# Optimization experiments

Measured on AMD Instinct MI355X. Metric: run time of the kernel, lower is better.

The kernel has to match this reference:

```python
import jax, jax.numpy as jnp
import numpy as np

TAU = 0.2  # temperature

def setup_inputs() -> dict:
    key = jax.random.key(0)
    k1, k2, k3 = jax.random.split(key, 3)
    query = jax.random.normal(k1, (8192, 128), dtype=jnp.float32)
    pos = jax.random.normal(k2, (8192, 128), dtype=jnp.float32)
    neg = jax.random.normal(k3, (16384, 128), dtype=jnp.float32)
    return {"query": query, "pos": pos, "neg": neg}

def reference(query, pos, neg):
    # scores: [N, M] = query @ neg^T / tau
    scores = jnp.einsum('nd,md->nm', query, neg) / TAU
    # positive logits: [N]
    pos_logit = jnp.sum(query * pos, axis=-1) / TAU
    # loss = mean_n( logsumexp_m(scores) - pos_logit )
    lse = jax.scipy.special.logsumexp(scores, axis=-1)
    return jnp.mean(lse - pos_logit)
```

## Files before the change

### kernel.cpp

```cpp
#include <hip/hip_runtime.h>
#include <cstdint>

#define NQ    8192
#define NNEG  16384
#define DIM   128
#define SPLIT 8
#define CHUNK (NNEG / SPLIT)
#define K_SCALE 7.2134752044448169f
#define LN2     0.69314718055994531f

typedef __attribute__((ext_vector_type(8))) __bf16 bf16x8;
typedef __attribute__((ext_vector_type(4))) float  f32x4;

__device__ inline void async_load16(const void* g, void* l) {
    __builtin_amdgcn_global_load_lds(
        (const __attribute__((address_space(1))) void*)g,
        (__attribute__((address_space(3))) void*)l, 16, 0, 0);
}

__device__ inline unsigned short f2bf(float x) {
    uint32_t u = __float_as_uint(x);
    u += 0x7fffu + ((u >> 16) & 1u);
    return (unsigned short)(u >> 16);
}

__device__ inline float waveReduceSum(float v) {
#pragma unroll
    for (int m = 32; m >= 1; m >>= 1) v += __shfl_xor(v, m, 64);
    return v;
}

__global__ __launch_bounds__(256) void iw_prep(
    const float* __restrict__ q, const float* __restrict__ neg,
    unsigned short* __restrict__ qb, unsigned short* __restrict__ nb,
    float* __restrict__ out)
{
    const int i = blockIdx.x * 256 + threadIdx.x;
    if (i == 0) out[0] = 0.f;
    constexpr int QG = NQ * DIM / 4;
    if (i < QG) {
        float4 v = ((const float4*)q)[i];
        ushort4 o;
        o.x = f2bf(v.x * K_SCALE); o.y = f2bf(v.y * K_SCALE);
        o.z = f2bf(v.z * K_SCALE); o.w = f2bf(v.w * K_SCALE);
        ((ushort4*)qb)[i] = o;
    } else {
        int j = i - QG;
        float4 v = ((const float4*)neg)[j];
        ushort4 o;
        o.x = f2bf(v.x); o.y = f2bf(v.y); o.z = f2bf(v.z); o.w = f2bf(v.w);
        ((ushort4*)nb)[j] = o;
    }
}

__global__ __launch_bounds__(256) void iw_pos(
    const float* __restrict__ q, const float* __restrict__ p,
    float* __restrict__ out)
{
    const int tid = threadIdx.x;
    float acc = 0.f;
    const float4* q4 = (const float4*)q;
    const float4* p4 = (const float4*)p;
    const int n4 = NQ * DIM / 4;
    for (int i = blockIdx.x * 256 + tid; i < n4; i += 128 * 256) {
        float4 a = q4[i], b = p4[i];
        acc = fmaf(a.x, b.x, fmaf(a.y, b.y, fmaf(a.z, b.z, fmaf(a.w, b.w, acc))));
    }
    acc = waveReduceSum(acc);
    __shared__ float red[4];
    if ((tid & 63) == 0) red[tid >> 6] = acc;
    __syncthreads();
    if (tid == 0) {
        float s = red[0] + red[1] + red[2] + red[3];
        atomicAdd(out, s * (-1.0f / (0.2f * (float)NQ)));
    }
}

__global__ __launch_bounds__(256, 2) void iw_main(
    const unsigned short* __restrict__ qb, const unsigned short* __restrict__ nb,
    float2* __restrict__ partial)
{
    constexpr int BM = 128, BN = 64, NIT = CHUNK / BN;
    __shared__ alignas(16) unsigned short q_lds[BM * DIM];
    __shared__ alignas(16) unsigned short n_lds[BN * DIM];

    const int tid  = threadIdx.x;
    const int lane = tid & 63;
    const int w    = tid >> 6;
    const int quad = lane >> 4;
    const int c0   = lane & 15;

    const int row0   = blockIdx.x * BM;
    const int nbase0 = blockIdx.y * CHUNK;

#pragma unroll
    for (int p = 0; p < 8; ++p) {
        int t   = w * 8 + p;
        int idx = t * 64 + lane;
        int r   = idx >> 4;
        int kb  = (idx & 15) ^ (r & 15);
        async_load16(qb + (size_t)(row0 + r) * DIM + kb * 8, q_lds + t * 512);
    }
    int nro[4], ndst[4];
#pragma unroll
    for (int p = 0; p < 4; ++p) {
        int t   = w * 4 + p;
        int idx = t * 64 + lane;
        int r   = idx >> 4;
        int kb  = (idx & 15) ^ (r & 15);
        nro[p]  = r * DIM + kb * 8;
        ndst[p] = t * 512;
        async_load16(nb + (size_t)nbase0 * DIM + nro[p], n_lds + ndst[p]);
    }
    __syncthreads();

    bf16x8 afrag[2][4];
#pragma unroll
    for (int rs = 0; rs < 2; ++rs)
#pragma unroll
        for (int ks = 0; ks < 4; ++ks) {
            int rl  = w * 32 + rs * 16 + c0;
            int blk = rl * 16 + ((ks * 4 + quad) ^ c0);
            afrag[rs][ks] = *reinterpret_cast<const bf16x8*>(q_lds + blk * 8);
        }

    float m_s[2][4], l_s[2][4];
#pragma unroll
    for (int rs = 0; rs < 2; ++rs)
#pragma unroll
        for (int i = 0; i < 4; ++i) { m_s[rs][i] = -1e30f; l_s[rs][i] = 0.f; }

    const f32x4 zero4 = {0.f, 0.f, 0.f, 0.f};

    for (int it = 0; it < NIT; ++it) {
        f32x4 acc[2][4];
#pragma unroll
        for (int rs = 0; rs < 2; ++rs)
#pragma unroll
            for (int ns = 0; ns < 4; ++ns) acc[rs][ns] = zero4;

#pragma unroll
        for (int ns = 0; ns < 4; ++ns) {
#pragma unroll
            for (int ks = 0; ks < 4; ++ks) {
                int blk = (ns * 16 + c0) * 16 + ((ks * 4 + quad) ^ c0);
                bf16x8 b = *reinterpret_cast<const bf16x8*>(n_lds + blk * 8);
                acc[0][ns] = __builtin_amdgcn_mfma_f32_16x16x32_bf16(afrag[0][ks], b, acc[0][ns], 0, 0, 0);
                acc[1][ns] = __builtin_amdgcn_mfma_f32_16x16x32_bf16(afrag[1][ks], b, acc[1][ns], 0, 0, 0);
            }
        }
        __syncthreads();
        if (it + 1 < NIT) {
            const unsigned short* src = nb + (size_t)(nbase0 + (it + 1) * BN) * DIM;
#pragma unroll
            for (int p = 0; p < 4; ++p) async_load16(src + nro[p], n_lds + ndst[p]);
        }
#pragma unroll
        for (int rs = 0; rs < 2; ++rs) {
#pragma unroll
            for (int i = 0; i < 4; ++i) {
                float y0 = acc[rs][0][i], y1 = acc[rs][1][i];
                float y2 = acc[rs][2][i], y3 = acc[rs][3][i];
                float mx = fmaxf(fmaxf(y0, y1), fmaxf(y2, y3));
                float m0 = m_s[rs][i];
                float nm = fmaxf(m0, mx);
                float t  = __builtin_amdgcn_exp2f(y0 - nm) + __builtin_amdgcn_exp2f(y1 - nm)
                         + __builtin_amdgcn_exp2f(y2 - nm) + __builtin_amdgcn_exp2f(y3 - nm);
                l_s[rs][i] = l_s[rs][i] * __builtin_amdgcn_exp2f(m0 - nm) + t;
                m_s[rs][i] = nm;
            }
        }
        __syncthreads();
    }

#pragma unroll
    for (int rs = 0; rs < 2; ++rs) {
#pragma unroll
        for (int i = 0; i < 4; ++i) {
            float m = m_s[rs][i], l = l_s[rs][i];
#pragma unroll
            for (int s = 1; s < 16; s <<= 1) {
                float om = __shfl_xor(m, s, 64);
                float ol = __shfl_xor(l, s, 64);
                float nm = fmaxf(m, om);
                l = l * __builtin_amdgcn_exp2f(m - nm) + ol * __builtin_amdgcn_exp2f(om - nm);
                m = nm;
            }
            if (c0 == 0) {
                int grow = row0 + w * 32 + rs * 16 + quad * 4 + i;
                partial[(size_t)blockIdx.y * NQ + grow] = make_float2(m, l);
            }
        }
    }
}

__global__ __launch_bounds__(256) void iw_merge(
    const float2* __restrict__ partial, float* __restrict__ out)
{
    const int tid = threadIdx.x;
    const int row = blockIdx.x * 256 + tid;
    float M = -1e30f, L = 0.f;
#pragma unroll
    for (int c = 0; c < SPLIT; ++c) {
        float2 p = partial[(size_t)c * NQ + row];
        float nm = fmaxf(M, p.x);
        L = L * __builtin_amdgcn_exp2f(M - nm) + p.y * __builtin_amdgcn_exp2f(p.x - nm);
        M = nm;
    }
    float lse = LN2 * (M + __log2f(L));
    float v = lse * (1.0f / (float)NQ);
    v = waveReduceSum(v);
    __shared__ float red[4];
    if ((tid & 63) == 0) red[tid >> 6] = v;
    __syncthreads();
    if (tid == 0) atomicAdd(out, red[0] + red[1] + red[2] + red[3]);
}

extern "C" void kernel_launch(void* const* d_in, const int* in_sizes, int n_in,
                              void* d_out, int out_size, void* d_ws, size_t ws_size,
                              hipStream_t stream) {
    const float* q   = (const float*)d_in[0];
    const float* pos = (const float*)d_in[1];
    const float* neg = (const float*)d_in[2];
    float* out = (float*)d_out;

    unsigned short* qb = (unsigned short*)d_ws;
    unsigned short* nb = qb + (size_t)NQ * DIM;
    float2* partial    = (float2*)(nb + (size_t)NNEG * DIM);

    iw_prep <<<3072, 256, 0, stream>>>(q, neg, qb, nb, out);
    iw_pos  <<<128,  256, 0, stream>>>(q, pos, out);
    iw_main <<<dim3(64, SPLIT), 256, 0, stream>>>(qb, nb, partial);
    iw_merge<<<32,   256, 0, stream>>>(partial, out);
}
```

Measured before the change: 121.8 us.

## Double-buffer negative tiles, drop Q LDS staging, fuse positive dot into prep

The main kernel now double-buffers the negative-tile LDS buffer, prefetching the next tile before the MFMA loop and keeping one barrier per iteration instead of two. Query fragments are loaded straight from global memory into registers, which frees the Q LDS buffer and lets the launch bound ask for 4 blocks per CU. The negative split count doubles to 16, giving more blocks and shorter chunks. The positive-logit dot product is fused into the bf16 conversion kernel, and the output is zeroed with a memset. The cost is more partials for the merge kernel to combine and uncoalesced direct-global Q fragment loads.

```diff
diff --git a/kernel.cpp b/kernel.cpp
--- a/kernel.cpp
+++ b/kernel.cpp
@@ -4,7 +4,7 @@
 #define NQ    8192
 #define NNEG  16384
 #define DIM   128
-#define SPLIT 8
+#define SPLIT 16
 #define CHUNK (NNEG / SPLIT)
 #define K_SCALE 7.2134752044448169f
 #define LN2     0.69314718055994531f
@@ -31,12 +31,13 @@
 }
 
 __global__ __launch_bounds__(256) void iw_prep(
-    const float* __restrict__ q, const float* __restrict__ neg,
+    const float* __restrict__ q, const float* __restrict__ p,
+    const float* __restrict__ neg,
     unsigned short* __restrict__ qb, unsigned short* __restrict__ nb,
     float* __restrict__ out)
 {
-    const int i = blockIdx.x * 256 + threadIdx.x;
-    if (i == 0) out[0] = 0.f;
+    const int tid = threadIdx.x;
+    const int i = blockIdx.x * 256 + tid;
     constexpr int QG = NQ * DIM / 4;
     if (i < QG) {
         float4 v = ((const float4*)q)[i];
@@ -44,6 +45,16 @@
         o.x = f2bf(v.x * K_SCALE); o.y = f2bf(v.y * K_SCALE);
         o.z = f2bf(v.z * K_SCALE); o.w = f2bf(v.w * K_SCALE);
         ((ushort4*)qb)[i] = o;
+        float4 pv = ((const float4*)p)[i];
+        float acc = fmaf(v.x, pv.x, fmaf(v.y, pv.y, fmaf(v.z, pv.z, v.w * pv.w)));
+        acc = waveReduceSum(acc);
+        __shared__ float red[4];
+        if ((tid & 63) == 0) red[tid >> 6] = acc;
+        __syncthreads();
+        if (tid == 0) {
+            float s = red[0] + red[1] + red[2] + red[3];
+            atomicAdd(out, s * (-1.0f / (0.2f * (float)NQ)));
+        }
     } else {
         int j = i - QG;
         float4 v = ((const float4*)neg)[j];
@@ -53,36 +64,12 @@
     }
 }
 
-__global__ __launch_bounds__(256) void iw_pos(
-    const float* __restrict__ q, const float* __restrict__ p,
-    float* __restrict__ out)
-{
-    const int tid = threadIdx.x;
-    float acc = 0.f;
-    const float4* q4 = (const float4*)q;
-    const float4* p4 = (const float4*)p;
-    const int n4 = NQ * DIM / 4;
-    for (int i = blockIdx.x * 256 + tid; i < n4; i += 128 * 256) {
-        float4 a = q4[i], b = p4[i];
-        acc = fmaf(a.x, b.x, fmaf(a.y, b.y, fmaf(a.z, b.z, fmaf(a.w, b.w, acc))));
-    }
-    acc = waveReduceSum(acc);
-    __shared__ float red[4];
-    if ((tid & 63) == 0) red[tid >> 6] = acc;
-    __syncthreads();
-    if (tid == 0) {
-        float s = red[0] + red[1] + red[2] + red[3];
-        atomicAdd(out, s * (-1.0f / (0.2f * (float)NQ)));
-    }
-}
-
-__global__ __launch_bounds__(256, 2) void iw_main(
+__global__ __launch_bounds__(256, 4) void iw_main(
     const unsigned short* __restrict__ qb, const unsigned short* __restrict__ nb,
     float2* __restrict__ partial)
 {
     constexpr int BM = 128, BN = 64, NIT = CHUNK / BN;
-    __shared__ alignas(16) unsigned short q_lds[BM * DIM];
-    __shared__ alignas(16) unsigned short n_lds[BN * DIM];
+    __shared__ alignas(16) unsigned short n_lds[2 * BN * DIM];
 
     const int tid  = threadIdx.x;
     const int lane = tid & 63;
@@ -93,46 +80,49 @@
     const int row0   = blockIdx.x * BM;
     const int nbase0 = blockIdx.y * CHUNK;
 
-#pragma unroll
-    for (int p = 0; p < 8; ++p) {
-        int t   = w * 8 + p;
+    bf16x8 afrag[2][4];
+#pragma unroll
+    for (int rs = 0; rs < 2; ++rs)
+#pragma unroll
+        for (int ks = 0; ks < 4; ++ks) {
+            const int qrow = row0 + w * 32 + rs * 16 + c0;
+            afrag[rs][ks] = *reinterpret_cast<const bf16x8*>(
+                qb + (size_t)qrow * DIM + ks * 32 + quad * 8);
+        }
+
+    int nro[4], ndst[4];
+#pragma unroll
+    for (int pp = 0; pp < 4; ++pp) {
+        int t   = w * 4 + pp;
         int idx = t * 64 + lane;
         int r   = idx >> 4;
         int kb  = (idx & 15) ^ (r & 15);
-        async_load16(qb + (size_t)(row0 + r) * DIM + kb * 8, q_lds + t * 512);
-    }
-    int nro[4], ndst[4];
-#pragma unroll
-    for (int p = 0; p < 4; ++p) {
-        int t   = w * 4 + p;
-        int idx = t * 64 + lane;
-        int r   = idx >> 4;
-        int kb  = (idx & 15) ^ (r & 15);
-        nro[p]  = r * DIM + kb * 8;
-        ndst[p] = t * 512;
-        async_load16(nb + (size_t)nbase0 * DIM + nro[p], n_lds + ndst[p]);
-    }
+        nro[pp]  = r * DIM + kb * 8;
+        ndst[pp] = t * 512;
+    }
+#pragma unroll
+    for (int pp = 0; pp < 4; ++pp)
+        async_load16(nb + (size_t)nbase0 * DIM + nro[pp], n_lds + ndst[pp]);
     __syncthreads();
 
-    bf16x8 afrag[2][4];
+    float m_s[2][4], l_s[2][4];
 #pragma unroll
     for (int rs = 0; rs < 2; ++rs)
 #pragma unroll
-        for (int ks = 0; ks < 4; ++ks) {
-            int rl  = w * 32 + rs * 16 + c0;
-            int blk = rl * 16 + ((ks * 4 + quad) ^ c0);
-            afrag[rs][ks] = *reinterpret_cast<const bf16x8*>(q_lds + blk * 8);
-        }
-
-    float m_s[2][4], l_s[2][4];
-#pragma unroll
-    for (int rs = 0; rs < 2; ++rs)
-#pragma unroll
         for (int i = 0; i < 4; ++i) { m_s[rs][i] = -1e30f; l_s[rs][i] = 0.f; }
 
     const f32x4 zero4 = {0.f, 0.f, 0.f, 0.f};
 
     for (int it = 0; it < NIT; ++it) {
+        const int buf  = (it & 1) * (BN * DIM);
+        if (it + 1 < NIT) {
+            const unsigned short* src = nb + (size_t)(nbase0 + (it + 1) * BN) * DIM;
+            const int nbuf = ((it + 1) & 1) * (BN * DIM);
+#pragma unroll
+            for (int pp = 0; pp < 4; ++pp)
+                async_load16(src + nro[pp], n_lds + nbuf + ndst[pp]);
+        }
+
         f32x4 acc[2][4];
 #pragma unroll
         for (int rs = 0; rs < 2; ++rs)
@@ -144,17 +134,12 @@
 #pragma unroll
             for (int ks = 0; ks < 4; ++ks) {
                 int blk = (ns * 16 + c0) * 16 + ((ks * 4 + quad) ^ c0);
-                bf16x8 b = *reinterpret_cast<const bf16x8*>(n_lds + blk * 8);
+                bf16x8 b = *reinterpret_cast<const bf16x8*>(n_lds + buf + blk * 8);
                 acc[0][ns] = __builtin_amdgcn_mfma_f32_16x16x32_bf16(afrag[0][ks], b, acc[0][ns], 0, 0, 0);
                 acc[1][ns] = __builtin_amdgcn_mfma_f32_16x16x32_bf16(afrag[1][ks], b, acc[1][ns], 0, 0, 0);
             }
         }
-        __syncthreads();
-        if (it + 1 < NIT) {
-            const unsigned short* src = nb + (size_t)(nbase0 + (it + 1) * BN) * DIM;
-#pragma unroll
-            for (int p = 0; p < 4; ++p) async_load16(src + nro[p], n_lds + ndst[p]);
-        }
+
 #pragma unroll
         for (int rs = 0; rs < 2; ++rs) {
 #pragma unroll
@@ -228,8 +213,8 @@
     unsigned short* nb = qb + (size_t)NQ * DIM;
     float2* partial    = (float2*)(nb + (size_t)NNEG * DIM);
 
-    iw_prep <<<3072, 256, 0, stream>>>(q, neg, qb, nb, out);
-    iw_pos  <<<128,  256, 0, stream>>>(q, pos, out);
-    iw_main <<<dim3(64, SPLIT), 256, 0, stream>>>(qb, nb, partial);
+    hipMemsetAsync(out, 0, sizeof(float), stream);
+    iw_prep <<<3072, 256, 0, stream>>>(q, pos, neg, qb, nb, out);
+    iw_main <<<dim3(NQ / 128, SPLIT), 256, 0, stream>>>(qb, nb, partial);
     iw_merge<<<32,   256, 0, stream>>>(partial, out);
 }
```

Result: slower. 133.0 us (+9.2%).
